# Kernel optimization log

Measured on AMD Instinct MI355X. Metric: run time of the kernel, lower is better.

Reference implementation:

```python
import jax, jax.numpy as jnp
import numpy as np

B, T, N, D = 32, 336, 321, 3
G = 512          # global_hidden
L = 2            # layer_nums
E = 4            # experts per layer
K = 2            # top-k
F = 2048         # d_ff (expert hidden)
P = 96           # pred_len
LOSS_COEF = 0.01


def setup_inputs() -> dict:
    key = jax.random.key(0)
    ks = iter(jax.random.split(key, 24))
    rn = lambda shape, s=0.02: jax.random.normal(next(ks), shape, jnp.float32) * s
    return {
        "x": jax.random.normal(next(ks), (B, T, N, D), jnp.float32),
        # GlobalEmbedding
        "Wv": rn((N, 1)), "bv": jnp.zeros((1,), jnp.float32),
        "Wt": rn((T, G)), "bt": jnp.zeros((G,), jnp.float32),
        # CrossAttention
        "Wq": rn((G, G)), "bq": jnp.zeros((G,), jnp.float32),
        "Wk": rn((G, G)), "bk": jnp.zeros((G,), jnp.float32),
        "Wva": rn((G, G)), "bva": jnp.zeros((G,), jnp.float32),
        # AMS MoE layers (stacked over L)
        "Wg": rn((L, T, E)),
        "We1": rn((L, E, T, F)), "be1": jnp.zeros((L, E, F), jnp.float32),
        "We2": rn((L, E, F, T)), "be2": jnp.zeros((L, E, T), jnp.float32),
        # projections head
        "P1w": rn((T, P)), "P1b": jnp.zeros((P,), jnp.float32),
        "P2w": rn((P, 2 * P)), "P2b": jnp.zeros((2 * P,), jnp.float32),
    }


def _cv_squared(v):
    return v.var() / (v.mean() ** 2 + 1e-10)


def reference(x, Wv, bv, Wt, bt, Wq, bq, Wk, bk, Wva, bva,
              Wg, We1, be1, We2, be2, P1w, P1b, P2w, P2b):
    Bv, Tv, Nv, Dv = x.shape
    # ---- GlobalEmbedding: (B,T,N,D) -> (B,D,G), with the original's raw reshape
    g = jnp.einsum('btvd,vo->btdo', x, Wv)[..., 0] + bv[0]        # (B,T,D)
    g2 = g.reshape(Bv * Dv, Tv) @ Wt + bt                          # faithful contiguous reshape
    gf = g2.reshape(Bv, Dv, -1)                                    # (B,D,G)
    # ---- CrossAttention (no sqrt(d) scaling, per source)
    q = gf @ Wq + bq
    kk = gf @ Wk + bk
    v = gf @ Wva + bva
    attn = jax.nn.softmax(jnp.einsum('big,bjg->bij', q, kk), axis=-1)
    sst_attended = jnp.einsum('bij,bjg->big', attn, v)[:, 0, :]    # unused: use_attend=0
    del sst_attended
    # ---- slice value channel + RevIN norm over time
    x0 = x[..., 0]                                                 # (B,T,N)
    mu = x0.mean(axis=1, keepdims=True)
    sd = jnp.sqrt(x0.var(axis=1, keepdims=True) + 1e-5)
    out = (x0 - mu) / sd
    # ---- AMS layers: clean top-k gated MoE over per-node seq MLP experts
    balance_loss = jnp.float32(0.0)
    for l in range(L):
        logits = out.mean(axis=2) @ Wg[l]                          # (B,E)
        topv, topi = jax.lax.top_k(logits, K)
        gates = jnp.zeros_like(logits).at[
            jnp.arange(Bv)[:, None], topi].set(jax.nn.softmax(topv, axis=-1))
        importance = gates.sum(axis=0)
        balance_loss = balance_loss + _cv_squared(importance) * LOSS_COEF
        xt = out.transpose(0, 2, 1)                                # (B,N,T)
        h = jax.nn.relu(jnp.einsum('bnt,etf->ebnf', xt, We1[l])
                        + be1[l][:, None, None, :])                # (E,B,N,F)
        eo = jnp.einsum('ebnf,eft->ebnt', h, We2[l]) + be2[l][:, None, None, :]
        moe = jnp.einsum('be,ebnt->bnt', gates, eo).transpose(0, 2, 1)
        out = out + moe                                            # residual_connection=1
    # ---- projection head
    o = out.transpose(0, 2, 1)                                     # (B,N,T)
    hproj = jnp.tanh(o @ P1w + P1b)
    p = (hproj @ P2w + P2b).reshape(Bv, Nv, P, 2).transpose(0, 2, 1, 3)  # (B,P,N,2)
    mean = p[..., 0]
    std = jax.nn.softplus(p[..., 1]) + 1e-6
    return mean, balance_loss, std
```

## Files before the change

kernel.cpp:

```cpp
#include <hip/hip_runtime.h>
#include <hip/hip_bf16.h>
#include <cstdint>
#include <math.h>

#define B_ 32
#define T_ 336
#define N_ 321
#define L_ 2
#define E_ 4
#define F_ 2048
#define P_ 96
#define TPAD 352
#define NPAD 384

typedef __hip_bfloat16 bf16;
typedef __attribute__((ext_vector_type(8))) __bf16 bf16x8;
typedef __attribute__((ext_vector_type(4))) float f32x4;


__device__ __forceinline__ void async_copy16(const void* g, void* l) {
  __builtin_amdgcn_global_load_lds(
      (__attribute__((address_space(1))) void*)(uintptr_t)g,
      (__attribute__((address_space(3))) void*)(unsigned int)(uintptr_t)l,
      16, 0, 0);
}

__device__ __forceinline__ void pipe_barrier_vm0() {
  asm volatile("s_waitcnt vmcnt(0)" ::: "memory");
  __builtin_amdgcn_s_barrier();
  __builtin_amdgcn_sched_barrier(0);
}

__device__ __forceinline__ void pipe_barrier_full() {
  asm volatile("s_waitcnt vmcnt(0) lgkmcnt(0)" ::: "memory");
  __builtin_amdgcn_s_barrier();
  __builtin_amdgcn_sched_barrier(0);
}

#define G2_WAITN(N)                                         \
  do {                                                      \
    asm volatile("s_waitcnt vmcnt(" #N ")" ::: "memory");   \
    __builtin_amdgcn_s_barrier();                           \
    __builtin_amdgcn_sched_barrier(0);                      \
  } while (0)

__global__ void transpose_cast_kernel(const float* __restrict__ src, bf16* __restrict__ dst,
                                      int R, int C, int Rp, int Cp,
                                      long long sStride, long long dStride) {
  __shared__ float tile[32][33];
  const float* s = src + (size_t)blockIdx.z * sStride;
  bf16* d = dst + (size_t)blockIdx.z * dStride;
  int r0 = blockIdx.x * 32, c0 = blockIdx.y * 32;
  int tx = threadIdx.x, ty = threadIdx.y;
  #pragma unroll
  for (int ii = 0; ii < 4; ii++) {
    int rl = ty * 4 + ii;
    int r = r0 + rl, c = c0 + tx;
    tile[rl][tx] = (r < R && c < C) ? s[(size_t)r * C + c] : 0.f;
  }
  __syncthreads();
  #pragma unroll
  for (int ii = 0; ii < 4; ii++) {
    int cl = ty * 4 + ii;
    int cd = c0 + cl, rd = r0 + tx;
    if (cd < Cp && rd < Rp)
      d[(size_t)cd * Rp + rd] = __float2bfloat16(tile[tx][cl]);
  }
}

__global__ void repack_w2_kernel(const float* __restrict__ src, bf16* __restrict__ dst) {
  __shared__ float tile[32][96];
  int le = blockIdx.z, tb = blockIdx.y, f0 = blockIdx.x * 32;
  int tid = threadIdx.x;
  const float* s = src + (size_t)le * F_ * T_;
  for (int idx = tid; idx < 32 * 96; idx += 256) {
    int ff = idx / 96, tt = idx % 96;
    int t = tb * 96 + tt;
    tile[ff][tt] = (t < T_) ? s[(size_t)(f0 + ff) * T_ + t] : 0.f;
  }
  __syncthreads();
  bf16* d = dst + ((size_t)le * 4 + tb) * 196608 + (size_t)(f0 >> 3) * 768;
  for (int s2 = tid; s2 < 384; s2 += 256) {
    int kgl = s2 / 96, row = s2 % 96;
    bf16 v[8];
    #pragma unroll
    for (int j = 0; j < 8; j++) v[j] = __float2bfloat16(tile[kgl * 8 + j][row]);
    *(uint4*)(d + (size_t)kgl * 768 + row * 8) = *(const uint4*)v;
  }
}

__global__ __launch_bounds__(512) void revin_kernel(const float* __restrict__ x,
                                                    float* __restrict__ out,
                                                    bf16* __restrict__ Abuf) {
  __shared__ float red[8][64][2];
  __shared__ float minv[64][2];
  __shared__ unsigned int Lt[64][177];

  const int b = blockIdx.x;
  const int n0 = blockIdx.y * 64;
  const int tid = threadIdx.x;
  const int nl = tid & 63, tq = tid >> 6;
  const int n = n0 + nl;
  const bool valid = (n < N_);
  const float* xp = x + ((size_t)b * T_ * N_ + n) * 3;
  const int tbeg = tq * 42, tend = tbeg + 42;

  float s1 = 0.f, s2 = 0.f;
  if (valid) {
    for (int t = tbeg; t < tend; t++) {
      float v = xp[(size_t)t * N_ * 3];
      s1 += v; s2 += v * v;
    }
  }
  red[tq][nl][0] = s1; red[tq][nl][1] = s2;
  __syncthreads();
  if (tid < 64) {
    float a = 0.f, c = 0.f;
    #pragma unroll
    for (int q = 0; q < 8; q++) { a += red[q][tid][0]; c += red[q][tid][1]; }
    float mu = a / (float)T_;
    float var = c / (float)T_ - mu * mu;
    minv[tid][0] = mu;
    minv[tid][1] = 1.f / sqrtf(var + 1e-5f);
  }
  {
    int r = tid >> 3, c = 168 + (tid & 7);
    Lt[r][c] = 0u;
  }
  __syncthreads();

  const float mu = minv[nl][0], inv = minv[nl][1];
  for (int t = tbeg; t < tend; t += 2) {
    float v0 = 0.f, v1 = 0.f;
    if (valid) {
      v0 = (xp[(size_t)t * N_ * 3] - mu) * inv;
      v1 = (xp[(size_t)(t + 1) * N_ * 3] - mu) * inv;
      out[((size_t)b * T_ + t) * N_ + n] = v0;
      out[((size_t)b * T_ + t + 1) * N_ + n] = v1;
    }
    bf16 h0 = __float2bfloat16(v0), h1 = __float2bfloat16(v1);
    unsigned int u = (unsigned int)*(unsigned short*)&h0 |
                     ((unsigned int)*(unsigned short*)&h1 << 16);
    Lt[nl][t >> 1] = u;
  }
  __syncthreads();

  unsigned int* abase = (unsigned int*)(Abuf + ((size_t)b * NPAD + n0) * TPAD);
  #pragma unroll
  for (int k = 0; k < 22; k++) {
    int idx = tid + k * 512;
    int row = idx / 176, c = idx % 176;
    abase[(size_t)row * (TPAD / 2) + c] = Lt[row][c];
  }
}

__global__ void gate1_kernel(const float* __restrict__ out, float* __restrict__ colsum) {
  int b = blockIdx.y;
  int w = threadIdx.x >> 6, lane = threadIdx.x & 63;
  int t = blockIdx.x * 16 + w * 4;
  #pragma unroll
  for (int i = 0; i < 4; i++, t++) {
    const float* p = out + ((size_t)b * T_ + t) * N_;
    float s = 0.f;
    for (int n = lane; n < N_; n += 64) s += p[n];
    #pragma unroll
    for (int off = 32; off; off >>= 1) s += __shfl_down(s, off);
    if (lane == 0) colsum[b * T_ + t] = s;
  }
}

__global__ void gate2_kernel(const float* __restrict__ colsum, const float* __restrict__ Wg,
                             int* __restrict__ pair_e, float* __restrict__ pair_gate,
                             float* __restrict__ loss_partial, int layer) {
  __shared__ float lg[32][4];
  __shared__ float gates[32][4];
  __shared__ float imp[4];
  int tid = threadIdx.x;
  if (tid < 128) {
    int b = tid >> 2, e = tid & 3;
    float s = 0.f;
    for (int t = 0; t < T_; t++)
      s += colsum[b * T_ + t] * Wg[(layer * T_ + t) * E_ + e];
    lg[b][e] = s / (float)N_;
  }
  __syncthreads();
  if (tid < 32) {
    float v[4];
    #pragma unroll
    for (int e = 0; e < 4; e++) v[e] = lg[tid][e];
    int i0 = 0;
    for (int e = 1; e < 4; e++) if (v[e] > v[i0]) i0 = e;
    int i1 = -1;
    for (int e = 0; e < 4; e++) {
      if (e == i0) continue;
      if (i1 < 0 || v[e] > v[i1]) i1 = e;
    }
    float ex = expf(v[i1] - v[i0]);
    float g0 = 1.f / (1.f + ex);
    float g1 = ex / (1.f + ex);
    pair_e[tid * 2] = i0; pair_e[tid * 2 + 1] = i1;
    pair_gate[tid * 2] = g0; pair_gate[tid * 2 + 1] = g1;
    #pragma unroll
    for (int e = 0; e < 4; e++) gates[tid][e] = 0.f;
    gates[tid][i0] = g0; gates[tid][i1] = g1;
  }
  __syncthreads();
  if (tid < 4) {
    float s = 0.f;
    for (int bb = 0; bb < 32; bb++) s += gates[bb][tid];
    imp[tid] = s;
  }
  __syncthreads();
  if (tid == 0) {
    float m = (imp[0] + imp[1] + imp[2] + imp[3]) * 0.25f;
    float va = 0.f;
    #pragma unroll
    for (int e = 0; e < 4; e++) { float d = imp[e] - m; va += d * d; }
    va *= 0.25f;
    loss_partial[layer] = 0.01f * (va / (m * m + 1e-10f));
  }
}

__global__ __launch_bounds__(256) void gemm1_kernel(
    const bf16* __restrict__ Abuf, const bf16* __restrict__ W1T,
    const float* __restrict__ be1, const int* __restrict__ pair_e,
    const float* __restrict__ pair_gate, bf16* __restrict__ h, int layer) {
  __shared__ __align__(16) bf16 S1[16384];
  __shared__ float bias_s[128];

  const int tid = threadIdx.x;
  const int w = tid >> 6, lane = tid & 63;
  const int pair = blockIdx.z;
  const int b = pair >> 1;
  const int e = pair_e[pair];
  const float gate = pair_gate[pair];
  const int m0 = blockIdx.y * 128;
  const int f0 = blockIdx.x * 128;

  const bf16* Ag = Abuf + (size_t)b * NPAD * TPAD + (size_t)m0 * TPAD;
  const bf16* Bg = W1T + ((size_t)(layer * E_ + e) * F_ + f0) * TPAD;
  if (tid < 128) bias_s[tid] = be1[(size_t)(layer * E_ + e) * F_ + f0 + tid];

  f32x4 acc[4][4];
  const f32x4 zero = {0.f, 0.f, 0.f, 0.f};
  #pragma unroll
  for (int i = 0; i < 4; i++)
    #pragma unroll
    for (int j = 0; j < 4; j++) acc[i][j] = zero;

  const int wm = w >> 1, wn = w & 1;
  const int lrow = lane >> 2;
  const int lkoff = (lane & 3) * 8;
  const int quad = lane >> 4;
  const int l15 = lane & 15;

  auto stage1 = [&](int k, int buf) {
    const int k0 = k * 32;
    bf16* As = S1 + buf * 8192;
    bf16* Bs = As + 4096;
    #pragma unroll
    for (int i = 0; i < 2; i++) {
      int r = (w * 2 + i) * 16 + lrow;
      async_copy16(Ag + (size_t)r * TPAD + k0 + lkoff, As + (w * 2 + i) * 512);
      async_copy16(Bg + (size_t)r * TPAD + k0 + lkoff, Bs + (w * 2 + i) * 512);
    }
  };

  stage1(0, 0);
  pipe_barrier_full();

  for (int kk = 0; kk < TPAD / 32; ++kk) {
    if (kk < TPAD / 32 - 1) stage1(kk + 1, (kk + 1) & 1);
    const bf16* As = S1 + (kk & 1) * 8192;
    const bf16* Bs = As + 4096;
    bf16x8 af[4], bfr[4];
    #pragma unroll
    for (int mi = 0; mi < 4; mi++)
      af[mi] = *(const bf16x8*)(As + (wm * 64 + mi * 16 + l15) * 32 + quad * 8);
    #pragma unroll
    for (int ni = 0; ni < 4; ni++)
      bfr[ni] = *(const bf16x8*)(Bs + (wn * 64 + ni * 16 + l15) * 32 + quad * 8);
    #pragma unroll
    for (int mi = 0; mi < 4; mi++)
      #pragma unroll
      for (int ni = 0; ni < 4; ni++)
        acc[mi][ni] = __builtin_amdgcn_mfma_f32_16x16x32_bf16(af[mi], bfr[ni], acc[mi][ni], 0, 0, 0);
    pipe_barrier_vm0();
  }

  bf16* tw0 = S1 + w * 1024;
  bf16* tw1 = S1 + 4096 + w * 1024;
  size_t hb = (size_t)pair * 786432 + (size_t)((m0 >> 6) + wm) * 131072;
  const int kgbase = (f0 >> 3) + wn * 8 + (lane & 3) * 2;
  #pragma unroll
  for (int mi = 0; mi < 4; mi++) {
    bf16* tw = (mi & 1) ? tw1 : tw0;
    #pragma unroll
    for (int ni = 0; ni < 4; ni++) {
      float bias = bias_s[wn * 64 + ni * 16 + l15];
      #pragma unroll
      for (int r = 0; r < 4; r++) {
        float v = acc[mi][ni][r] + bias;
        v = fmaxf(v, 0.f) * gate;
        tw[(quad * 4 + r) * 64 + ni * 16 + l15] = __float2bfloat16(v);
      }
    }
    int row = lane >> 2;
    int fpart = (lane & 3) * 16;
    const uint4* sp = (const uint4*)(tw + row * 64 + fpart);
    uint4 d0 = sp[0];
    uint4 d1 = sp[1];
    bf16* dp = h + hb + (size_t)kgbase * 512 + (mi * 16 + row) * 8;
    *(uint4*)dp = d0;
    *(uint4*)(dp + 512) = d1;
  }
}

#define CT_STRIDE 104
__global__ __launch_bounds__(256) void gemm2_kernel(
    const bf16* __restrict__ h, const bf16* __restrict__ W2B,
    const float* __restrict__ be2, const int* __restrict__ pair_e,
    const float* __restrict__ pair_gate, float* __restrict__ out,
    bf16* __restrict__ Abuf, int layer) {
  __shared__ __align__(16) bf16 S[24576];
  __shared__ float bias_t[96];

  const int tid = threadIdx.x;
  const int w = tid >> 6, lane = tid & 63;
  const int id = blockIdx.x;
  const int u = id & 7;
  const int v = id >> 3;
  const int tt = v & 3;
  const int pn = u + 8 * (v >> 2);
  const int b = pn / 6, nt = pn % 6;
  const int n0 = nt * 64, t0 = tt * 96;

  const int e0 = pair_e[b * 2], e1 = pair_e[b * 2 + 1];
  const float g0 = pair_gate[b * 2], g1 = pair_gate[b * 2 + 1];
  const bf16* Agb0 = h + ((size_t)(b * 2) * 6 + nt) * 131072;
  const bf16* Agb1 = h + ((size_t)(b * 2 + 1) * 6 + nt) * 131072;
  const bf16* Bgb0 = W2B + ((size_t)(layer * E_ + e0) * 4 + tt) * 196608;
  const bf16* Bgb1 = W2B + ((size_t)(layer * E_ + e1) * 4 + tt) * 196608;
  const int quad = lane >> 4, l15 = lane & 15;
  const int wm = w >> 1, wt = w & 1;

  if (tid < 96) {
    int t = t0 + tid;
    bias_t[tid] = (t < T_)
        ? g0 * be2[(layer * E_ + e0) * T_ + t] + g1 * be2[(layer * E_ + e1) * T_ + t]
        : 0.f;
  }
  pipe_barrier_full();

  f32x4 acc[2][3];
  const f32x4 zero = {0.f, 0.f, 0.f, 0.f};
  #pragma unroll
  for (int i = 0; i < 2; i++)
    #pragma unroll
    for (int jj = 0; jj < 3; jj++) acc[i][jj] = zero;

  const int aoff = w * 1024 + lane * 8;
  const int boff = w * 1536 + lane * 8;

  auto stageA = [&](const bf16* Aj, int buf) {
    bf16* As2 = S + buf * 4096;
    async_copy16(Aj + aoff, As2 + w * 1024);
    async_copy16(Aj + aoff + 512, As2 + w * 1024 + 512);
  };
  auto stageB = [&](const bf16* Bj, int buf) {
    bf16* Bs2 = S + 12288 + buf * 6144;
    async_copy16(Bj + boff, Bs2 + w * 1536);
    async_copy16(Bj + boff + 512, Bs2 + w * 1536 + 512);
    async_copy16(Bj + boff + 1024, Bs2 + w * 1536 + 1024);
  };

  auto compute = [&](int bufA, int bufB) {
    const bf16* As2 = S + bufA * 4096;
    const bf16* Bs2 = S + 12288 + bufB * 6144;
    #pragma unroll
    for (int w32 = 0; w32 < 2; w32++) {
      const int kg = w32 * 4 + quad;
      bf16x8 af[2], bfr[3];
      #pragma unroll
      for (int mi = 0; mi < 2; mi++)
        af[mi] = *(const bf16x8*)(As2 + kg * 512 + (wm * 32 + mi * 16 + l15) * 8);
      #pragma unroll
      for (int ni = 0; ni < 3; ni++)
        bfr[ni] = *(const bf16x8*)(Bs2 + kg * 768 + (wt * 48 + ni * 16 + l15) * 8);
      #pragma unroll
      for (int mi = 0; mi < 2; mi++)
        #pragma unroll
        for (int ni = 0; ni < 3; ni++)
          acc[mi][ni] = __builtin_amdgcn_mfma_f32_16x16x32_bf16(af[mi], bfr[ni], acc[mi][ni], 0, 0, 0);
    }
  };

  stageB(Bgb0, 0);
  stageA(Agb0, 0);
  stageA(Agb0 + 4096, 1);
  G2_WAITN(2);

  const bf16* aNext = Agb0 + 2 * 4096;
  const bf16* bNext = Bgb0 + 6144;

  #pragma unroll 1
  for (int j = 0; j < 10; ++j) {
    const int k = j * 6;
#define G2S(i, bB1, bA2, cA, cB)                              \
    stageB(bNext, bB1);                                       \
    stageA(aNext, bA2);                                       \
    bNext = (k + (i) == 30) ? Bgb1 : bNext + 6144;            \
    aNext = (k + (i) == 29) ? Agb1 : aNext + 4096;            \
    compute(cA, cB);                                          \
    G2_WAITN(2);
    G2S(0, 1, 2, 0, 0)
    G2S(1, 0, 0, 1, 1)
    G2S(2, 1, 1, 2, 0)
    G2S(3, 0, 2, 0, 1)
    G2S(4, 1, 0, 1, 0)
    G2S(5, 0, 1, 2, 1)
#undef G2S
  }

  stageB(bNext, 1);
  stageA(aNext, 2);
  bNext += 6144; aNext += 4096;
  compute(0, 0);
  G2_WAITN(2);

  stageB(bNext, 0);
  stageA(aNext, 0);
  bNext += 6144;
  compute(1, 1);
  G2_WAITN(2);

  stageB(bNext, 1);
  compute(2, 0);
  G2_WAITN(0);

  compute(0, 1);
  pipe_barrier_full();

  #pragma unroll
  for (int mi = 0; mi < 2; mi++) {
    #pragma unroll
    for (int ni = 0; ni < 3; ni++) {
      int nloc_b = wm * 32 + mi * 16 + quad * 4;
      int tloc = wt * 48 + ni * 16 + l15;
      int t = t0 + tloc;
      #pragma unroll
      for (int r = 0; r < 4; r++) {
        int nloc = nloc_b + r;
        int n = n0 + nloc;
        float vv = 0.f;
        if (n < N_ && t < T_) {
          size_t q = ((size_t)b * T_ + t) * N_ + n;
          vv = out[q] + acc[mi][ni][r] + bias_t[tloc];
          out[q] = vv;
        }
        S[nloc * CT_STRIDE + tloc] = __float2bfloat16(vv);
      }
    }
  }
  __syncthreads();
  #pragma unroll
  for (int it = 0; it < 3; ++it) {
    int idx = tid + it * 256;
    int row = idx / 12, seg = idx % 12;
    int t = t0 + seg * 8;
    if (t < TPAD)
      *(uint4*)(Abuf + ((size_t)b * NPAD + n0 + row) * TPAD + t) =
          *(const uint4*)(S + row * CT_STRIDE + seg * 8);
  }
}

#define HS_STRIDE 104
__global__ __launch_bounds__(256) void proj_kernel(
    const bf16* __restrict__ Abuf, const bf16* __restrict__ P1T, const float* __restrict__ P1b,
    const bf16* __restrict__ P2T, const float* __restrict__ P2b,
    const float* __restrict__ loss_partial, float* __restrict__ dout) {
  __shared__ __align__(16) bf16 Hs[64 * HS_STRIDE];
  const int tid = threadIdx.x;
  const int w = tid >> 6, lane = tid & 63;
  const int quad = lane >> 4, l15 = lane & 15;
  const int b = blockIdx.y;
  const int m0 = blockIdx.x * 64;
  const int row = w * 16;

  f32x4 acc1[6];
  const f32x4 zero = {0.f, 0.f, 0.f, 0.f};
  #pragma unroll
  for (int j = 0; j < 6; j++) acc1[j] = zero;

  const bf16* Arow = Abuf + ((size_t)b * NPAD + m0 + row) * TPAD;
  for (int kk = 0; kk < TPAD / 32; ++kk) {
    bf16x8 af, bfr[6];
    af = *(const bf16x8*)(Arow + (size_t)l15 * TPAD + kk * 32 + quad * 8);
    #pragma unroll
    for (int ni = 0; ni < 6; ni++)
      bfr[ni] = *(const bf16x8*)(P1T + (size_t)(ni * 16 + l15) * TPAD + kk * 32 + quad * 8);
    #pragma unroll
    for (int ni = 0; ni < 6; ni++)
      acc1[ni] = __builtin_amdgcn_mfma_f32_16x16x32_bf16(af, bfr[ni], acc1[ni], 0, 0, 0);
  }

  #pragma unroll
  for (int ni = 0; ni < 6; ni++) {
    float bias = P1b[ni * 16 + l15];
    #pragma unroll
    for (int r = 0; r < 4; r++) {
      float x = acc1[ni][r] + bias;
      float t = 1.f - 2.f / (__expf(2.f * x) + 1.f);
      Hs[(row + quad * 4 + r) * HS_STRIDE + ni * 16 + l15] = __float2bfloat16(t);
    }
  }
  __syncthreads();

  #pragma unroll
  for (int half = 0; half < 2; ++half) {
    f32x4 acc2[6];
    #pragma unroll
    for (int j = 0; j < 6; j++) acc2[j] = zero;

    #pragma unroll
    for (int kk = 0; kk < 3; ++kk) {
      bf16x8 af, bfr[6];
      af = *(const bf16x8*)(Hs + (row + l15) * HS_STRIDE + kk * 32 + quad * 8);
      #pragma unroll
      for (int ni = 0; ni < 6; ni++)
        bfr[ni] = *(const bf16x8*)(P2T + (size_t)((half * 6 + ni) * 16 + l15) * P_ + kk * 32 + quad * 8);
      #pragma unroll
      for (int ni = 0; ni < 6; ni++)
        acc2[ni] = __builtin_amdgcn_mfma_f32_16x16x32_bf16(af, bfr[ni], acc2[ni], 0, 0, 0);
    }

    #pragma unroll
    for (int ni = 0; ni < 6; ni++) {
      int jj = (half * 6 + ni) * 16 + l15;
      float bias = P2b[jj];
      int pout = jj >> 1;
      #pragma unroll
      for (int r = 0; r < 4; r++) {
        int n = m0 + row + quad * 4 + r;
        if (n < N_) {
          float s = acc2[ni][r] + bias;
          size_t o = ((size_t)b * P_ + pout) * N_ + n;
          if ((jj & 1) == 0) {
            dout[o] = s;
          } else {
            float sp = (s > 20.f) ? s : log1pf(__expf(s));
            dout[(size_t)B_ * P_ * N_ + 1 + o] = sp + 1e-6f;
          }
        }
      }
    }
  }
  if (b == 0 && blockIdx.x == 0 && tid == 0)
    dout[(size_t)B_ * P_ * N_] = loss_partial[0] + loss_partial[1];
}

extern "C" void kernel_launch(void* const* d_in, const int* in_sizes, int n_in,
                              void* d_out, int out_size, void* d_ws, size_t ws_size,
                              hipStream_t stream) {
  const float* x   = (const float*)d_in[0];
  const float* Wg  = (const float*)d_in[11];
  const float* We1 = (const float*)d_in[12];
  const float* be1 = (const float*)d_in[13];
  const float* We2 = (const float*)d_in[14];
  const float* be2 = (const float*)d_in[15];
  const float* P1w = (const float*)d_in[16];
  const float* P1b = (const float*)d_in[17];
  const float* P2w = (const float*)d_in[18];
  const float* P2b = (const float*)d_in[19];

  char* ws = (char*)d_ws;
  size_t off = 0;
  auto alloc = [&](size_t bytes) -> void* {
    void* p = ws + off;
    off += (bytes + 255) & ~(size_t)255;
    return p;
  };
  float* out        = (float*)alloc((size_t)B_ * T_ * N_ * 4);
  bf16*  Abuf       = (bf16*) alloc((size_t)B_ * NPAD * TPAD * 2);
  bf16*  W1T        = (bf16*) alloc((size_t)L_ * E_ * F_ * TPAD * 2);
  bf16*  W2B        = (bf16*) alloc((size_t)L_ * E_ * 4 * 196608 * 2);
  bf16*  P1T        = (bf16*) alloc((size_t)P_ * TPAD * 2);
  bf16*  P2T        = (bf16*) alloc((size_t)2 * P_ * P_ * 2);
  bf16*  h          = (bf16*) alloc((size_t)B_ * 2 * 786432 * 2);
  float* colsum     = (float*)alloc((size_t)B_ * T_ * 4);
  int*   pair_e     = (int*)  alloc(B_ * 2 * 4);
  float* pair_gate  = (float*)alloc(B_ * 2 * 4);
  float* loss_part  = (float*)alloc(2 * 4);
  if (ws_size < off) return;

  dim3 tb(32, 8);
  transpose_cast_kernel<<<dim3(11, 64, 8), tb, 0, stream>>>(
      We1, W1T, T_, F_, TPAD, F_, (long long)T_ * F_, (long long)F_ * TPAD);
  repack_w2_kernel<<<dim3(64, 4, 8), 256, 0, stream>>>(We2, W2B);
  transpose_cast_kernel<<<dim3(11, 3, 1), tb, 0, stream>>>(
      P1w, P1T, T_, P_, TPAD, P_, 0, 0);
  transpose_cast_kernel<<<dim3(3, 6, 1), tb, 0, stream>>>(
      P2w, P2T, P_, 2 * P_, P_, 2 * P_, 0, 0);

  revin_kernel<<<dim3(B_, 6), 512, 0, stream>>>(x, out, Abuf);

  for (int l = 0; l < L_; ++l) {
    gate1_kernel<<<dim3(21, B_), 256, 0, stream>>>(out, colsum);
    gate2_kernel<<<1, 128, 0, stream>>>(colsum, Wg, pair_e, pair_gate, loss_part, l);
    gemm1_kernel<<<dim3(16, 3, 64), 256, 0, stream>>>(Abuf, W1T, be1, pair_e, pair_gate, h, l);
    gemm2_kernel<<<768, 256, 0, stream>>>(h, W2B, be2, pair_e, pair_gate, out, Abuf, l);
  }

  proj_kernel<<<dim3(6, B_), 256, 0, stream>>>(Abuf, P1T, P1b, P2T, P2b, loss_part,
                                               (float*)d_out);
}
```

Baseline: 504.4 us.

## Fuse MoE gating into GEMM kernels and compute column sums in producer epilogues

Removes the separate gate1/gate2 kernels per layer. Column sums over N are accumulated with atomics in the revin kernel and, for layer 0, in the gemm2 epilogue. Each GEMM block then recomputes the gate logits, top-2 selection and gate weights redundantly from those sums, and one block computes the balance loss. This saves four kernel launches and one full read of the activation tensor per layer. In exchange it adds per-block gating arithmetic, float atomics with nondeterministic summation order, and a memset.

Measured after the change: 496.4 us. Within noise of the previous version (-1.6%).

```diff
diff --git a/kernel.cpp b/kernel.cpp
--- a/kernel.cpp
+++ b/kernel.cpp
@@ -44,6 +44,78 @@
     __builtin_amdgcn_sched_barrier(0);                      \
   } while (0)
 
+__device__ __forceinline__ void gate_logits(const float* __restrict__ cs,
+                                            const float* __restrict__ Wg,
+                                            int layer, int b, float* lgs, int tid) {
+  if (tid < 64) {
+    const int e = tid & 3, toff = tid >> 2;
+    float s = 0.f;
+    for (int j = 0; j < 21; j++) {
+      int t = toff + (j << 4);
+      s += cs[b * T_ + t] * Wg[(layer * T_ + t) * E_ + e];
+    }
+    #pragma unroll
+    for (int m = 4; m < 64; m <<= 1) s += __shfl_xor(s, m);
+    if (tid < 4) lgs[tid] = s / (float)N_;
+  }
+}
+
+__device__ __forceinline__ void top2_from(const float* lgs, int& i0, int& i1,
+                                          float& g0, float& g1) {
+  float v[4] = {lgs[0], lgs[1], lgs[2], lgs[3]};
+  i0 = 0;
+  for (int e = 1; e < 4; e++) if (v[e] > v[i0]) i0 = e;
+  i1 = -1;
+  for (int e = 0; e < 4; e++) {
+    if (e == i0) continue;
+    if (i1 < 0 || v[e] > v[i1]) i1 = e;
+  }
+  float ex = expf(v[i1] - v[i0]);
+  g0 = 1.f / (1.f + ex);
+  g1 = ex / (1.f + ex);
+}
+
+__device__ __forceinline__ void balance_loss(const float* __restrict__ cs,
+                                             const float* __restrict__ Wg,
+                                             int layer, int lane,
+                                             float* __restrict__ loss_partial) {
+  float gg0 = 0.f, gg1 = 0.f, gg2 = 0.f, gg3 = 0.f;
+  if (lane < 32) {
+    const int bb = lane;
+    float s0 = 0.f, s1 = 0.f, s2 = 0.f, s3 = 0.f;
+    for (int t = 0; t < T_; t++) {
+      float c = cs[bb * T_ + t];
+      const float* wr = Wg + (size_t)(layer * T_ + t) * E_;
+      s0 += c * wr[0]; s1 += c * wr[1]; s2 += c * wr[2]; s3 += c * wr[3];
+    }
+    float v[4] = {s0 / (float)N_, s1 / (float)N_, s2 / (float)N_, s3 / (float)N_};
+    int i0 = 0;
+    for (int e = 1; e < 4; e++) if (v[e] > v[i0]) i0 = e;
+    int i1 = -1;
+    for (int e = 0; e < 4; e++) {
+      if (e == i0) continue;
+      if (i1 < 0 || v[e] > v[i1]) i1 = e;
+    }
+    float ex = expf(v[i1] - v[i0]);
+    float a = 1.f / (1.f + ex), q = ex / (1.f + ex);
+    gg0 = (i0 == 0) ? a : ((i1 == 0) ? q : 0.f);
+    gg1 = (i0 == 1) ? a : ((i1 == 1) ? q : 0.f);
+    gg2 = (i0 == 2) ? a : ((i1 == 2) ? q : 0.f);
+    gg3 = (i0 == 3) ? a : ((i1 == 3) ? q : 0.f);
+  }
+  #pragma unroll
+  for (int m = 1; m < 32; m <<= 1) {
+    gg0 += __shfl_xor(gg0, m); gg1 += __shfl_xor(gg1, m);
+    gg2 += __shfl_xor(gg2, m); gg3 += __shfl_xor(gg3, m);
+  }
+  if (lane == 0) {
+    float mm = (gg0 + gg1 + gg2 + gg3) * 0.25f;
+    float d0 = gg0 - mm, d1 = gg1 - mm, d2 = gg2 - mm, d3 = gg3 - mm;
+    float va = (d0 * d0 + d1 * d1 + d2 * d2 + d3 * d3) * 0.25f;
+    loss_partial[layer] = 0.01f * (va / (mm * mm + 1e-10f));
+  }
+}
+
 __global__ void transpose_cast_kernel(const float* __restrict__ src, bf16* __restrict__ dst,
                                       int R, int C, int Rp, int Cp,
                                       long long sStride, long long dStride) {
@@ -91,7 +163,8 @@
 
 __global__ __launch_bounds__(512) void revin_kernel(const float* __restrict__ x,
                                                     float* __restrict__ out,
-                                                    bf16* __restrict__ Abuf) {
+                                                    bf16* __restrict__ Abuf,
+                                                    float* __restrict__ cs0) {
   __shared__ float red[8][64][2];
   __shared__ float minv[64][2];
   __shared__ unsigned int Lt[64][177];
@@ -138,6 +211,16 @@
       out[((size_t)b * T_ + t) * N_ + n] = v0;
       out[((size_t)b * T_ + t + 1) * N_ + n] = v1;
     }
+    float c0 = v0, c1 = v1;
+    #pragma unroll
+    for (int m = 1; m < 64; m <<= 1) {
+      c0 += __shfl_xor(c0, m);
+      c1 += __shfl_xor(c1, m);
+    }
+    if (nl == 0) {
+      atomicAdd(cs0 + b * T_ + t, c0);
+      atomicAdd(cs0 + b * T_ + t + 1, c1);
+    }
     bf16 h0 = __float2bfloat16(v0), h1 = __float2bfloat16(v1);
     unsigned int u = (unsigned int)*(unsigned short*)&h0 |
                      ((unsigned int)*(unsigned short*)&h1 << 16);
@@ -154,88 +237,30 @@
   }
 }
 
-__global__ void gate1_kernel(const float* __restrict__ out, float* __restrict__ colsum) {
-  int b = blockIdx.y;
-  int w = threadIdx.x >> 6, lane = threadIdx.x & 63;
-  int t = blockIdx.x * 16 + w * 4;
-  #pragma unroll
-  for (int i = 0; i < 4; i++, t++) {
-    const float* p = out + ((size_t)b * T_ + t) * N_;
-    float s = 0.f;
-    for (int n = lane; n < N_; n += 64) s += p[n];
-    #pragma unroll
-    for (int off = 32; off; off >>= 1) s += __shfl_down(s, off);
-    if (lane == 0) colsum[b * T_ + t] = s;
-  }
-}
-
-__global__ void gate2_kernel(const float* __restrict__ colsum, const float* __restrict__ Wg,
-                             int* __restrict__ pair_e, float* __restrict__ pair_gate,
-                             float* __restrict__ loss_partial, int layer) {
-  __shared__ float lg[32][4];
-  __shared__ float gates[32][4];
-  __shared__ float imp[4];
-  int tid = threadIdx.x;
-  if (tid < 128) {
-    int b = tid >> 2, e = tid & 3;
-    float s = 0.f;
-    for (int t = 0; t < T_; t++)
-      s += colsum[b * T_ + t] * Wg[(layer * T_ + t) * E_ + e];
-    lg[b][e] = s / (float)N_;
-  }
-  __syncthreads();
-  if (tid < 32) {
-    float v[4];
-    #pragma unroll
-    for (int e = 0; e < 4; e++) v[e] = lg[tid][e];
-    int i0 = 0;
-    for (int e = 1; e < 4; e++) if (v[e] > v[i0]) i0 = e;
-    int i1 = -1;
-    for (int e = 0; e < 4; e++) {
-      if (e == i0) continue;
-      if (i1 < 0 || v[e] > v[i1]) i1 = e;
-    }
-    float ex = expf(v[i1] - v[i0]);
-    float g0 = 1.f / (1.f + ex);
-    float g1 = ex / (1.f + ex);
-    pair_e[tid * 2] = i0; pair_e[tid * 2 + 1] = i1;
-    pair_gate[tid * 2] = g0; pair_gate[tid * 2 + 1] = g1;
-    #pragma unroll
-    for (int e = 0; e < 4; e++) gates[tid][e] = 0.f;
-    gates[tid][i0] = g0; gates[tid][i1] = g1;
-  }
-  __syncthreads();
-  if (tid < 4) {
-    float s = 0.f;
-    for (int bb = 0; bb < 32; bb++) s += gates[bb][tid];
-    imp[tid] = s;
-  }
-  __syncthreads();
-  if (tid == 0) {
-    float m = (imp[0] + imp[1] + imp[2] + imp[3]) * 0.25f;
-    float va = 0.f;
-    #pragma unroll
-    for (int e = 0; e < 4; e++) { float d = imp[e] - m; va += d * d; }
-    va *= 0.25f;
-    loss_partial[layer] = 0.01f * (va / (m * m + 1e-10f));
-  }
-}
-
 __global__ __launch_bounds__(256) void gemm1_kernel(
     const bf16* __restrict__ Abuf, const bf16* __restrict__ W1T,
-    const float* __restrict__ be1, const int* __restrict__ pair_e,
-    const float* __restrict__ pair_gate, bf16* __restrict__ h, int layer) {
+    const float* __restrict__ be1, const float* __restrict__ cs,
+    const float* __restrict__ Wg, float* __restrict__ loss_partial,
+    bf16* __restrict__ h, int layer) {
   __shared__ __align__(16) bf16 S1[16384];
   __shared__ float bias_s[128];
+  __shared__ float lgs[4];
 
   const int tid = threadIdx.x;
   const int w = tid >> 6, lane = tid & 63;
   const int pair = blockIdx.z;
   const int b = pair >> 1;
-  const int e = pair_e[pair];
-  const float gate = pair_gate[pair];
   const int m0 = blockIdx.y * 128;
   const int f0 = blockIdx.x * 128;
+
+  gate_logits(cs, Wg, layer, b, lgs, tid);
+  if (blockIdx.x == 0 && blockIdx.y == 0 && pair == 0 && w == 1)
+    balance_loss(cs, Wg, layer, lane, loss_partial);
+  __syncthreads();
+  int i0, i1; float ga, gb;
+  top2_from(lgs, i0, i1, ga, gb);
+  const int e = __builtin_amdgcn_readfirstlane((pair & 1) ? i1 : i0);
+  const float gate = (pair & 1) ? gb : ga;
 
   const bf16* Ag = Abuf + (size_t)b * NPAD * TPAD + (size_t)m0 * TPAD;
   const bf16* Bg = W1T + ((size_t)(layer * E_ + e) * F_ + f0) * TPAD;
@@ -319,11 +344,13 @@
 #define CT_STRIDE 104
 __global__ __launch_bounds__(256) void gemm2_kernel(
     const bf16* __restrict__ h, const bf16* __restrict__ W2B,
-    const float* __restrict__ be2, const int* __restrict__ pair_e,
-    const float* __restrict__ pair_gate, float* __restrict__ out,
-    bf16* __restrict__ Abuf, int layer) {
+    const float* __restrict__ be2, const float* __restrict__ cs_cur,
+    float* __restrict__ cs_next, const float* __restrict__ Wg,
+    float* __restrict__ out, bf16* __restrict__ Abuf, int layer) {
   __shared__ __align__(16) bf16 S[24576];
   __shared__ float bias_t[96];
+  __shared__ float lgs[4];
+  __shared__ float csl[96];
 
   const int tid = threadIdx.x;
   const int w = tid >> 6, lane = tid & 63;
@@ -335,8 +362,14 @@
   const int b = pn / 6, nt = pn % 6;
   const int n0 = nt * 64, t0 = tt * 96;
 
-  const int e0 = pair_e[b * 2], e1 = pair_e[b * 2 + 1];
-  const float g0 = pair_gate[b * 2], g1 = pair_gate[b * 2 + 1];
+  gate_logits(cs_cur, Wg, layer, b, lgs, tid);
+  if (tid < 96) csl[tid] = 0.f;
+  __syncthreads();
+  int i0, i1; float g0, g1;
+  top2_from(lgs, i0, i1, g0, g1);
+  const int e0 = __builtin_amdgcn_readfirstlane(i0);
+  const int e1 = __builtin_amdgcn_readfirstlane(i1);
+
   const bf16* Agb0 = h + ((size_t)(b * 2) * 6 + nt) * 131072;
   const bf16* Agb1 = h + ((size_t)(b * 2 + 1) * 6 + nt) * 131072;
   const bf16* Bgb0 = W2B + ((size_t)(layer * E_ + e0) * 4 + tt) * 196608;
@@ -441,6 +474,7 @@
   compute(0, 1);
   pipe_barrier_full();
 
+  float ps[3] = {0.f, 0.f, 0.f};
   #pragma unroll
   for (int mi = 0; mi < 2; mi++) {
     #pragma unroll
@@ -458,9 +492,15 @@
           vv = out[q] + acc[mi][ni][r] + bias_t[tloc];
           out[q] = vv;
         }
+        ps[ni] += vv;
         S[nloc * CT_STRIDE + tloc] = __float2bfloat16(vv);
       }
     }
+  }
+  if (layer == 0) {
+    #pragma unroll
+    for (int ni = 0; ni < 3; ni++)
+      atomicAdd(&csl[wt * 48 + ni * 16 + l15], ps[ni]);
   }
   __syncthreads();
   #pragma unroll
@@ -471,6 +511,10 @@
     if (t < TPAD)
       *(uint4*)(Abuf + ((size_t)b * NPAD + n0 + row) * TPAD + t) =
           *(const uint4*)(S + row * CT_STRIDE + seg * 8);
+  }
+  if (layer == 0 && tid < 96) {
+    int t = t0 + tid;
+    if (t < T_) atomicAdd(cs_next + b * T_ + t, csl[tid]);
   }
 }
 
@@ -587,9 +631,7 @@
   bf16*  P1T        = (bf16*) alloc((size_t)P_ * TPAD * 2);
   bf16*  P2T        = (bf16*) alloc((size_t)2 * P_ * P_ * 2);
   bf16*  h          = (bf16*) alloc((size_t)B_ * 2 * 786432 * 2);
-  float* colsum     = (float*)alloc((size_t)B_ * T_ * 4);
-  int*   pair_e     = (int*)  alloc(B_ * 2 * 4);
-  float* pair_gate  = (float*)alloc(B_ * 2 * 4);
+  float* colsum     = (float*)alloc((size_t)2 * B_ * T_ * 4);
   float* loss_part  = (float*)alloc(2 * 4);
   if (ws_size < off) return;
 
@@ -602,13 +644,15 @@
   transpose_cast_kernel<<<dim3(3, 6, 1), tb, 0, stream>>>(
       P2w, P2T, P_, 2 * P_, P_, 2 * P_, 0, 0);
 
-  revin_kernel<<<dim3(B_, 6), 512, 0, stream>>>(x, out, Abuf);
+  hipMemsetAsync(colsum, 0, (size_t)2 * B_ * T_ * 4, stream);
+  revin_kernel<<<dim3(B_, 6), 512, 0, stream>>>(x, out, Abuf, colsum);
 
   for (int l = 0; l < L_; ++l) {
-    gate1_kernel<<<dim3(21, B_), 256, 0, stream>>>(out, colsum);
-    gate2_kernel<<<1, 128, 0, stream>>>(colsum, Wg, pair_e, pair_gate, loss_part, l);
-    gemm1_kernel<<<dim3(16, 3, 64), 256, 0, stream>>>(Abuf, W1T, be1, pair_e, pair_gate, h, l);
-    gemm2_kernel<<<768, 256, 0, stream>>>(h, W2B, be2, pair_e, pair_gate, out, Abuf, l);
+    const float* cs = colsum + (size_t)l * B_ * T_;
+    gemm1_kernel<<<dim3(16, 3, 64), 256, 0, stream>>>(
+        Abuf, W1T, be1, cs, Wg, loss_part, h, l);
+    gemm2_kernel<<<768, 256, 0, stream>>>(
+        h, W2B, be2, cs, colsum + (size_t)B_ * T_, Wg, out, Abuf, l);
   }
 
   proj_kernel<<<dim3(6, B_), 256, 0, stream>>>(Abuf, P1T, P1b, P2T, P2b, loss_part,
```
